# Kernel tuning notes

Hardware: AMD Instinct MI355X
Metric: run time of the kernel (lower is better)

The kernel has to match this reference:

```python
import jax, jax.numpy as jnp
import numpy as np

B, E, W, HID, HOR = 16, 128, 256, 64, 12
EPS = 1e-5


def conv1d(x, w, b, stride=1, padding=0, groups=1):
    # x: [N, Cin, L], w: [Cout, Cin//groups, K]
    y = jax.lax.conv_general_dilated(x, w, (stride,), [(padding, padding)],
                                     feature_group_count=groups,
                                     dimension_numbers=('NCH', 'OIH', 'NCH'))
    return y + b[None, :, None]


def setup_inputs() -> dict:
    key = jax.random.key(0)
    ks = jax.random.split(key, 20)
    def rn(k, shape, scale):
        return jax.random.normal(k, shape, dtype=jnp.float32) * scale
    return {
        'x': rn(ks[0], (B, 1, W), 1.0),
        'noise': rn(ks[1], (HOR, B * E), 1.0),
        'affine_weight': jnp.ones((E,), jnp.float32),
        'affine_bias': jnp.zeros((E,), jnp.float32),
        'pe_w1': rn(ks[2], (32, 1, 5), 1.0 / np.sqrt(5.0)),
        'pe_b1': jnp.zeros((32,), jnp.float32),
        'bn_gamma': jnp.ones((32,), jnp.float32),
        'bn_beta': jnp.zeros((32,), jnp.float32),
        'bn_mean': jnp.zeros((32,), jnp.float32),
        'bn_var': jnp.ones((32,), jnp.float32),
        'pe_w2': rn(ks[3], (E, 32, 1), 1.0 / np.sqrt(32.0)),
        'pe_b2': jnp.zeros((E,), jnp.float32),
        'net_w1': rn(ks[4], (E, 64, 1, 2), 1.0 / np.sqrt(2.0)),
        'net_b1': jnp.zeros((E, 64), jnp.float32),
        'net_w2': rn(ks[5], (E, 64, 4, 2), 1.0 / np.sqrt(8.0)),
        'net_b2': jnp.zeros((E, 64), jnp.float32),
        'net_w3': rn(ks[6], (E, 1, 64, 1), 1.0 / np.sqrt(64.0)),
        'net_b3': jnp.zeros((E, 1), jnp.float32),
        'gat_wl': rn(ks[7], (HID, HID), 1.0 / np.sqrt(HID)),
        'gat_bl': jnp.zeros((HID,), jnp.float32),
        'gat_wr': rn(ks[8], (HID, HID), 1.0 / np.sqrt(HID)),
        'gat_br': jnp.zeros((HID,), jnp.float32),
        'gat_attn': rn(ks[9], (HID,), 1.0 / np.sqrt(HID)),
        'out_w': rn(ks[10], (E, HID), 1.0 / np.sqrt(HID)),
        'out_b': jnp.zeros((E,), jnp.float32),
        'ce_w': rn(ks[11], (HID, 3), 1.0 / np.sqrt(3.0)),
        'ce_b': jnp.zeros((HID,), jnp.float32),
        'cd_w': rn(ks[12], (4, HID), 1.0 / np.sqrt(HID)),
        'cd_b': jnp.zeros((4,), jnp.float32),
        'q_w': rn(ks[13], (32, W), 1.0 / np.sqrt(W)),
        'q_b': jnp.zeros((32,), jnp.float32),
        'k_w': rn(ks[14], (32, W), 1.0 / np.sqrt(W)),
        'k_b': jnp.zeros((32,), jnp.float32),
    }


def reference(x, noise, affine_weight, affine_bias, pe_w1, pe_b1, bn_gamma, bn_beta,
              bn_mean, bn_var, pe_w2, pe_b2, net_w1, net_b1, net_w2, net_b2, net_w3,
              net_b3, gat_wl, gat_bl, gat_wr, gat_br, gat_attn, out_w, out_b,
              ce_w, ce_b, cd_w, cd_b, q_w, q_b, k_w, k_b):
    # instance norm over time axis (unbiased=False, no eps, as in the torch code)
    mean = jnp.mean(x, axis=2, keepdims=True)              # [B,1,1]
    std = jnp.sqrt(jnp.var(x, axis=2, keepdims=True))
    xn = (x - mean) / std

    # path_encoder: conv(1->32,k5,p2) + ReLU + BN(eval) + conv(32->E,k1)
    h0 = jax.nn.relu(conv1d(xn, pe_w1, pe_b1, padding=2))
    h0 = (h0 - bn_mean[None, :, None]) / jnp.sqrt(bn_var + EPS)[None, :, None]
    h0 = h0 * bn_gamma[None, :, None] + bn_beta[None, :, None]
    xf = conv1d(h0, pe_w2, pe_b2)                          # [B,E,W]
    xf = xf * affine_weight[None, :, None] + affine_bias[None, :, None]

    # adjacency learner: softmax(Q K^T) over nodes, then hard threshold
    q = jnp.einsum('bew,hw->beh', xf, q_w) + q_b           # [B,E,32]
    k = jnp.einsum('bew,hw->beh', xf, k_w) + k_b
    adj_soft = jax.nn.softmax(jnp.einsum('bih,bjh->bij', q, k), axis=-1)  # [B,E,E]
    adj_bin = (adj_soft > 0.5).astype(jnp.float32)

    def cnn1d(xc, w1, b1, w2, b2, w3, b3):
        # xc: [B,1,W] -> [B,1,HID]; kernel=stride=down_factor//2=2
        h1 = jnp.tanh(conv1d(xc, w1, b1, stride=2))
        h2 = jnp.tanh(conv1d(h1, w2, b2, stride=2, groups=16))
        return jnp.tanh(conv1d(h2, w3, b3))

    vcnn = jax.vmap(cnn1d, in_axes=(0, 0, 0, 0, 0, 0, 0))

    def gat(h, adj):
        # GATv2, single head, is_concat: e[b,i,j] = a^T lrelu(g_r[i]+g_l[j])
        gl = jnp.einsum('bnf,of->bno', h, gat_wl) + gat_bl   # [B,N,HID]
        gr = jnp.einsum('bnf,of->bno', h, gat_wr) + gat_br
        gs = gr[:, :, None, :] + gl[:, None, :, :]           # [B,N,N,HID]
        e = jnp.einsum('bijf,f->bij', jax.nn.leaky_relu(gs, 0.2), gat_attn)
        e = jnp.where(adj == 0, jnp.float32(-1e20), e)
        a = jax.nn.softmax(e, axis=2)
        return jnp.einsum('bij,bjf->bif', a, gr)             # [B,N,HID]

    def mech(Q_t, P_t, adj, nz):
        Hh, Ee, Vv = Q_t[:, 0], Q_t[:, 1], Q_t[:, 2]
        al, be, ga, et = P_t[:, 0], P_t[:, 1], P_t[:, 2], P_t[:, 3]
        E_coup = jnp.einsum('bij,bj->bi', adj, Ee.reshape(B, E)).reshape(B * E)
        H_new = Hh - al * Hh
        E_new = Ee + be * Hh - ga * Ee + 0.1 * E_coup
        V_new = Vv + et * Ee + nz * 0.01
        return jnp.stack([H_new, E_new, V_new], axis=1)

    Q0 = jnp.tile(jnp.array([1.0, 0.0, 0.0], jnp.float32), (B * E, 1))

    def step(carry, nz):
        xc, Q_t = carry
        xper = xc.transpose(1, 0, 2)[:, :, None, :]          # [E,B,1,W]
        h = vcnn(xper, net_w1, net_b1, net_w2, net_b2, net_w3, net_b3)
        h = h[:, :, 0, :].transpose(1, 0, 2)                 # [B,E,HID]
        h_temp = gat(h, adj_bin)
        H_causal = jnp.tanh(Q_t @ ce_w.T + ce_b).reshape(B, E, HID)
        h = h + jnp.tanh(h_temp) + H_causal
        x_pred = jnp.einsum('beh,eh->be', h, out_w) + out_b  # grouped conv == per-node dot
        x_new = jnp.concatenate([xc[:, :, 1:], x_pred[:, :, None]], axis=2)
        P_t = jax.nn.sigmoid(h.reshape(B * E, HID) @ cd_w.T + cd_b)
        Q_new = mech(Q_t, P_t, adj_bin, nz)
        return (x_new, Q_new), (x_pred, P_t)

    (_, Q_final), (x_preds, P_all) = jax.lax.scan(step, (xf, Q0), noise)
    x_pred_all = x_preds.transpose(1, 2, 0)                  # [B,E,HOR]
    out = (x_pred_all - affine_bias[None, :, None]) / affine_weight[None, :, None]
    out = out * std + mean
    return out, Q_final.reshape(B, E, 3), P_all[-1].reshape(B, E, 4), adj_soft
```

## Files before the change

kernel.cpp:

```cpp
#include <hip/hip_runtime.h>


typedef __attribute__((ext_vector_type(4))) float f32x4;

struct Params {
  const float *__restrict__ x, *__restrict__ noise, *__restrict__ aw, *__restrict__ ab,
              *__restrict__ pe_w1, *__restrict__ pe_b1, *__restrict__ bn_g, *__restrict__ bn_b,
              *__restrict__ bn_m, *__restrict__ bn_v, *__restrict__ pe_w2, *__restrict__ pe_b2,
              *__restrict__ w1, *__restrict__ b1, *__restrict__ w2, *__restrict__ b2,
              *__restrict__ w3, *__restrict__ b3, *__restrict__ wl, *__restrict__ bl,
              *__restrict__ wr, *__restrict__ br, *__restrict__ attn, *__restrict__ out_w,
              *__restrict__ out_b, *__restrict__ ce_w, *__restrict__ ce_b, *__restrict__ cd_w,
              *__restrict__ cd_b, *__restrict__ q_w, *__restrict__ q_b, *__restrict__ k_w,
              *__restrict__ k_b;
  float* ws;
  float* out;
};

__device__ __forceinline__ float fast_tanh(float x) {
  float t = exp2f(fminf(2.8853900818f * x, 126.0f));
  return 1.0f - 2.0f * __builtin_amdgcn_rcpf(t + 1.0f);
}
__device__ __forceinline__ float fast_sigmoid(float x) {
  float t = exp2f(fminf(-1.44269504f * x, 126.0f));
  return __builtin_amdgcn_rcpf(1.0f + t);
}
__device__ __forceinline__ float wsum(float v) {
  #pragma unroll
  for (int m = 1; m < 64; m <<= 1) v += __shfl_xor(v, m, 64);
  return v;
}
__device__ __forceinline__ float wmax(float v) {
  #pragma unroll
  for (int m = 1; m < 64; m <<= 1) v = fmaxf(v, __shfl_xor(v, m, 64));
  return v;
}
__device__ __forceinline__ float load_llc(const float* p) {
  return __hip_atomic_load(p, __ATOMIC_RELAXED, __HIP_MEMORY_SCOPE_AGENT);
}
__device__ __forceinline__ void store_llc(float* p, float v) {
  __hip_atomic_store(p, v, __ATOMIC_RELAXED, __HIP_MEMORY_SCOPE_AGENT);
}
__device__ __forceinline__ f32x4 load_llc4(const float* p) {
  f32x4 v;
  asm volatile("global_load_dwordx4 %0, %1, off sc0 sc1" : "=v"(v) : "v"(p));
  return v;
}
__device__ __forceinline__ float load_llc1(const float* p) {
  float v;
  asm volatile("global_load_dword %0, %1, off sc0 sc1" : "=v"(v) : "v"(p));
  return v;
}
__device__ __forceinline__ void lds_fence() {
  asm volatile("s_waitcnt lgkmcnt(0)" ::: "memory");
  __builtin_amdgcn_sched_barrier(0);
}

#define OFF_MS   0
#define OFF_EB   32
#define OFF_CNT  4128
#define OFF_QV   16416
#define OFF_KV   81952
#define OFF_GL   147488
#define OFF_GR   409632
#define OFF_H0   671776
#define OFF_XW   802848
#define OFF_G    1359904

__global__ __launch_bounds__(256)
void k1_h0(Params P) {
  __shared__ float red[8];
  const int tid = threadIdx.x, blk = blockIdx.x;
  const int idx = blk * 256 + tid;
  const int b = idx >> 13, c = (idx >> 8) & 31, w = idx & 255;
  const int lane = tid & 63, wv = tid >> 6;

  float v = P.x[b * 256 + w];
  float s = wsum(v), s2 = wsum(v * v);
  if (lane == 0) { red[wv] = s; red[4 + wv] = s2; }
  __syncthreads();
  float st  = red[0] + red[1] + red[2] + red[3];
  float st2 = red[4] + red[5] + red[6] + red[7];
  float mean = st * (1.f / 256.f);
  float var  = st2 * (1.f / 256.f) - mean * mean;
  float sd   = sqrtf(var);
  float* ms = P.ws + OFF_MS;
  if (tid == 0) { ms[b] = mean; ms[16 + b] = sd; }

  float rstd = 1.f / sd;
  float acc = P.pe_b1[c];
  #pragma unroll
  for (int k = 0; k < 5; k++) {
    int u = w - 2 + k;
    float xv = (u >= 0 && u < 256) ? (P.x[b * 256 + u] - mean) * rstd : 0.f;
    acc += P.pe_w1[c * 5 + k] * xv;
  }
  acc = fmaxf(acc, 0.f);
  float sc = P.bn_g[c] / sqrtf(P.bn_v[c] + 1e-5f);
  (P.ws + OFF_H0)[idx] = (acc - P.bn_m[c]) * sc + P.bn_b[c];
}

__global__ __launch_bounds__(256)
void k2_xf(Params P) {
  const int idx = blockIdx.x * 256 + threadIdx.x;
  const int b = idx >> 15, e = (idx >> 8) & 127, w = idx & 255;
  const float* w2p  = P.pe_w2 + e * 32;
  const float* hcol = P.ws + OFF_H0 + b * 8192 + w;
  float acc = P.pe_b2[e];
  #pragma unroll 8
  for (int c = 0; c < 32; c++) acc += w2p[c] * hcol[c * 256];
  acc = acc * P.aw[e] + P.ab[e];
  (P.ws + OFF_XW)[(b * 128 + e) * 272 + w] = acc;
}

__global__ __launch_bounds__(256)
void k3_G(Params P) {
  const int row = blockIdx.x;
  const int es  = row & 127;
  const int s   = threadIdx.x;
  const float* w1p = P.w1 + es * 128;
  const float* w2p = P.w2 + es * 512;
  const float* w3p = P.w3 + es * 64;
  const float* b1p = P.b1 + es * 64;
  const float* b2p = P.b2 + es * 64;
  const float  b3v = P.b3[es];
  const float* xr  = P.ws + OFF_XW + row * 272;
  if (s >= 253) return;
  float X0 = xr[s], X1 = xr[s + 1], X2 = xr[s + 2], X3 = xr[s + 3];
  float acc = 0.f;
  #pragma unroll 1
  for (int g2 = 0; g2 < 16; g2++) {
    float h1v[8];
    #pragma unroll
    for (int ic = 0; ic < 4; ic++) {
      int ch = g2 * 4 + ic;
      float ww0 = w1p[ch * 2], ww1 = w1p[ch * 2 + 1], bb = b1p[ch];
      h1v[ic * 2 + 0] = fast_tanh(bb + ww0 * X0 + ww1 * X1);
      h1v[ic * 2 + 1] = fast_tanh(bb + ww0 * X2 + ww1 * X3);
    }
    #pragma unroll
    for (int oc = 0; oc < 4; oc++) {
      int ch = g2 * 4 + oc;
      const float* wq = w2p + ch * 8;
      float a2 = b2p[ch];
      #pragma unroll
      for (int u = 0; u < 8; u++) a2 += wq[u] * h1v[u];
      acc += w3p[ch] * fast_tanh(a2);
    }
  }
  (P.ws + OFF_G)[row * 272 + s] = fast_tanh(b3v + acc);
}

__global__ __launch_bounds__(256)
void k4_qk(Params P) {
  const int gtid = blockIdx.x * 256 + threadIdx.x;
  if (gtid < 16) ((int*)(P.ws + OFF_CNT))[gtid * 32] = 0;
  const int half = gtid >> 16;
  const int idx  = gtid & 65535;
  const int row  = idx >> 5, h = idx & 31;
  const float* wm  = half ? P.k_w : P.q_w;
  const float* bv  = half ? P.k_b : P.q_b;
  const float* xr  = P.ws + OFF_XW + row * 272;
  const float* wrw = wm + h * 256;
  float acc = bv[h];
  #pragma unroll 8
  for (int w = 0; w < 256; w += 4) {
    float4 xx = *(const float4*)(xr + w);
    float4 wq = *(const float4*)(wrw + w);
    acc += xx.x * wq.x + xx.y * wq.y + xx.z * wq.z + xx.w * wq.w;
  }
  ((half ? P.ws + OFF_KV : P.ws + OFF_QV))[idx] = acc;
}

__global__ __launch_bounds__(1024, 4)
void k_scan(Params P) {
  __shared__ __align__(16) float glS_[8192];
  __shared__ __align__(16) float grTS_[8192];
  __shared__ __align__(16) float WlS_[4096];
  __shared__ __align__(16) float WrS_[4096];
  __shared__ __align__(16) float wscb[16 * 336];
  __shared__ __align__(16) float attnS[64];
  const int tid = threadIdx.x, lane = tid & 63, wv = tid >> 6;
  const int row = blockIdx.x * 16 + wv;
  const int b = row >> 7, e = row & 127;
  float* ws = P.ws;
  float* abuf = wscb + wv * 336;
  float* hb   = abuf + 128;
  float* h1b  = abuf + 192;
  float* hist = abuf + 320;
  const float4* hb4   = (const float4*)hb;
  const float4* abuf4 = (const float4*)abuf;
  const float4* attn4 = (const float4*)attnS;
  char* glS  = (char*)glS_;
  char* grTS = (char*)grTS_;
  char* WlSc = (char*)WlS_;
  char* WrSc = (char*)WrS_;
  const float* grow_G = ws + OFF_G + row * 272;
  int* cntb = (int*)(ws + OFF_CNT) + b * 32;

  {
    int o = tid >> 4, q = tid & 15;
    float4 vl = *(const float4*)(P.wl + o * 64 + q * 4);
    float4 vr = *(const float4*)(P.wr + o * 64 + q * 4);
    int off = o * 256 + ((q ^ (o & 15)) << 4);
    *(float4*)(WlSc + off) = vl;
    *(float4*)(WrSc + off) = vr;
  }
  if (tid < 64) attnS[tid] = P.attn[tid];

  float cew0 = P.ce_w[lane * 3], cew1 = P.ce_w[lane * 3 + 1], cew2 = P.ce_w[lane * 3 + 2];
  float cebv = P.ce_b[lane];
  float cdw0 = P.cd_w[lane], cdw1 = P.cd_w[64 + lane], cdw2 = P.cd_w[128 + lane], cdw3 = P.cd_w[192 + lane];
  float cdb0 = P.cd_b[0], cdb1 = P.cd_b[1], cdb2 = P.cd_b[2], cdb3 = P.cd_b[3];
  float outw = P.out_w[e * 64 + lane], outb = P.out_b[e];
  float blv = P.bl[lane], brv = P.br[lane];
  float awv = P.aw[e], abv = P.ab[e];
  float meanb = ws[OFF_MS + b], stdb = ws[OFF_MS + 16 + b];
  float w10 = P.w1[e * 128 + lane * 2], w11 = P.w1[e * 128 + lane * 2 + 1];
  float b1v = P.b1[e * 64 + lane], b2v = P.b2[e * 64 + lane];
  float w3v = P.w3[e * 64 + lane], b3c = P.b3[e];
  float w2r[8];
  {
    const float4* w24 = (const float4*)(P.w2 + e * 512 + lane * 8);
    float4 a = w24[0], c = w24[1];
    w2r[0] = a.x; w2r[1] = a.y; w2r[2] = a.z; w2r[3] = a.w;
    w2r[4] = c.x; w2r[5] = c.y; w2r[6] = c.z; w2r[7] = c.w;
  }

  bool a0b, a1b;
  {
    if (lane < 32) hb[lane] = (ws + OFF_QV)[row * 32 + lane];
    lds_fence();
    float e0, e1;
    #pragma unroll
    for (int half = 0; half < 2; half++) {
      int j = lane + half * 64;
      const float* kr = ws + OFF_KV + (b * 128 + j) * 32;
      float acc = 0.f;
      #pragma unroll
      for (int h = 0; h < 32; h += 4) {
        float4 kk = *(const float4*)(kr + h);
        float4 qq = *(const float4*)(hb + h);
        acc += qq.x * kk.x + qq.y * kk.y + qq.z * kk.z + qq.w * kk.w;
      }
      if (half == 0) e0 = acc; else e1 = acc;
    }
    float m   = wmax(fmaxf(e0, e1));
    float p0  = __expf(e0 - m), p1 = __expf(e1 - m);
    float inv = 1.f / wsum(p0 + p1);
    float av0 = p0 * inv, av1 = p1 * inv;
    P.out[38912 + row * 128 + lane]      = av0;
    P.out[38912 + row * 128 + lane + 64] = av1;
    a0b = av0 > 0.5f; a1b = av1 > 0.5f;
  }

  float h_own = grow_G[4 * lane];
  float xA = (ws + OFF_XW)[row * 272 + 253];
  float xB = (ws + OFF_XW)[row * 272 + 254];
  float xC = (ws + OFF_XW)[row * 272 + 255];
  float q0 = 1.f, q1 = 0.f, q2 = 0.f;
  if (lane == 0) store_llc(ws + OFF_EB + row, 0.f);

  __syncthreads();

  hb[lane] = h_own;
  lds_fence();
  float gri;
  {
    float glx = blv, grx = brv;
    const int k = lane & 15;
    #pragma unroll
    for (int q = 0; q < 16; q++) {
      float4 hq  = hb4[q];
      float4 wl4 = *(const float4*)(WlSc + lane * 256 + ((q ^ k) << 4));
      float4 wr4 = *(const float4*)(WrSc + lane * 256 + ((q ^ k) << 4));
      glx += hq.x * wl4.x + hq.y * wl4.y + hq.z * wl4.z + hq.w * wl4.w;
      grx += hq.x * wr4.x + hq.y * wr4.y + hq.z * wr4.z + hq.w * wr4.w;
    }
    store_llc(ws + OFF_GL + row * 64 + lane, glx);
    store_llc(ws + OFF_GR + b * 8192 + lane * 128 + e, grx);
    gri = grx;
  }

  #pragma unroll 1
  for (int t = 0; t < 12; t++) {
    asm volatile("s_waitcnt vmcnt(0)" ::: "memory");
    __syncthreads();
    if (tid == 0) {
      __hip_atomic_fetch_add(cntb, 1, __ATOMIC_RELAXED, __HIP_MEMORY_SCOPE_AGENT);
      const int target = (t + 1) * 8;
      while (__hip_atomic_load(cntb, __ATOMIC_RELAXED, __HIP_MEMORY_SCOPE_AGENT) < target)
        __builtin_amdgcn_s_sleep(2);
    }
    __syncthreads();

    const float* glG   = ws + OFF_GL + (t & 1) * 131072 + b * 8192;
    const float* grTG  = ws + OFF_GR + (t & 1) * 131072 + b * 8192;
    const float* EbO   = ws + OFF_EB + (t & 1) * 2048;
    float*       EbN   = ws + OFF_EB + ((t + 1) & 1) * 2048;
    float*       glGn  = ws + OFF_GL + ((t + 1) & 1) * 131072;
    float*       grTGn = ws + OFF_GR + ((t + 1) & 1) * 131072;

    float ebv0 = load_llc1(EbO + b * 128 + lane);
    float ebv1 = load_llc1(EbO + b * 128 + lane + 64);
    const int jj0 = tid >> 4, cc0 = tid & 15;
    const int jj1 = 64 + jj0;
    const int ff0 = tid >> 5, dd0 = tid & 31;
    const int ff1 = 32 + ff0;
    f32x4 vg0 = load_llc4(glG  + jj0 * 64  + cc0 * 4);
    f32x4 vg1 = load_llc4(glG  + jj1 * 64  + cc0 * 4);
    f32x4 vr0 = load_llc4(grTG + ff0 * 128 + dd0 * 4);
    f32x4 vr1 = load_llc4(grTG + ff1 * 128 + dd0 * 4);

    asm volatile("s_waitcnt vmcnt(2)" ::: "memory");
    __builtin_amdgcn_sched_barrier(0);
    *(f32x4*)(glS + jj0 * 256 + ((cc0 ^ (jj0 & 15)) << 4)) = vg0;
    *(f32x4*)(glS + jj1 * 256 + ((cc0 ^ (jj1 & 15)) << 4)) = vg1;
    hb[lane] = gri;
    asm volatile("s_waitcnt lgkmcnt(0)" ::: "memory");
    __builtin_amdgcn_sched_barrier(0);
    __builtin_amdgcn_s_barrier();

    float ev0 = 0.f, ev1 = 0.f;
    {
      const char* r0 = glS + lane * 256;
      const char* r1 = glS + (lane + 64) * 256;
      const int k = lane & 15;
      #pragma unroll
      for (int c = 0; c < 16; c++) {
        float4 hq = hb4[c];
        float4 aq = attn4[c];
        int off = (c ^ k) << 4;
        float4 g0 = *(const float4*)(r0 + off);
        float4 g1 = *(const float4*)(r1 + off);
        float v;
        v = hq.x + g0.x; ev0 += fmaxf(v, 0.2f * v) * aq.x;
        v = hq.y + g0.y; ev0 += fmaxf(v, 0.2f * v) * aq.y;
        v = hq.z + g0.z; ev0 += fmaxf(v, 0.2f * v) * aq.z;
        v = hq.w + g0.w; ev0 += fmaxf(v, 0.2f * v) * aq.w;
        v = hq.x + g1.x; ev1 += fmaxf(v, 0.2f * v) * aq.x;
        v = hq.y + g1.y; ev1 += fmaxf(v, 0.2f * v) * aq.y;
        v = hq.z + g1.z; ev1 += fmaxf(v, 0.2f * v) * aq.z;
        v = hq.w + g1.w; ev1 += fmaxf(v, 0.2f * v) * aq.w;
      }
    }

    asm volatile("s_waitcnt vmcnt(0)" ::: "memory");
    __builtin_amdgcn_sched_barrier(0);
    *(f32x4*)(grTS + ff0 * 512 + ((dd0 ^ (ff0 & 15)) << 4)) = vr0;
    *(f32x4*)(grTS + ff1 * 512 + ((dd0 ^ (ff1 & 15)) << 4)) = vr1;

    ev0 = a0b ? ev0 : -1e20f;
    ev1 = a1b ? ev1 : -1e20f;
    float m   = wmax(fmaxf(ev0, ev1));
    float p0  = __expf(ev0 - m), p1 = __expf(ev1 - m);
    float inv = 1.f / wsum(p0 + p1);
    abuf[lane]      = p0 * inv;
    abuf[lane + 64] = p1 * inv;
    __syncthreads();

    float ht = 0.f;
    {
      const char* rr = grTS + lane * 512;
      const int k = lane & 15;
      #pragma unroll
      for (int c = 0; c < 32; c++) {
        float4 aq = abuf4[c];
        float4 g  = *(const float4*)(rr + ((c ^ k) << 4));
        ht += aq.x * g.x + aq.y * g.y + aq.z * g.z + aq.w * g.w;
      }
    }

    float hc = fast_tanh(cebv + q0 * cew0 + q1 * cew1 + q2 * cew2);
    float hf = h_own + fast_tanh(ht) + hc;

    float xp = wsum(hf * outw) + outb;
    float d0 = wsum(hf * cdw0);
    float d1 = wsum(hf * cdw1);
    float d2 = wsum(hf * cdw2);
    float d3 = wsum(hf * cdw3);
    float al = fast_sigmoid(d0 + cdb0);
    float be = fast_sigmoid(d1 + cdb1);
    float ga = fast_sigmoid(d2 + cdb2);
    float et = fast_sigmoid(d3 + cdb3);

    float ec = (a0b ? ebv0 : 0.f) + (a1b ? ebv1 : 0.f);
    ec = wsum(ec);

    float Hn = q0 - al * q0;
    float En = q1 + be * q0 - ga * q1 + 0.1f * ec;
    float Vn = q2 + et * q1 + P.noise[t * 2048 + row] * 0.01f;
    q0 = Hn; q1 = En; q2 = Vn;
    if (lane == 0) {
      store_llc(EbN + row, En);
      P.out[row * 12 + t] = (xp - abv) / awv * stdb + meanb;
      if (t == 11) {
        P.out[24576 + row * 3]     = Hn;
        P.out[24576 + row * 3 + 1] = En;
        P.out[24576 + row * 3 + 2] = Vn;
        P.out[30720 + row * 4]     = al;
        P.out[30720 + row * 4 + 1] = be;
        P.out[30720 + row * 4 + 2] = ga;
        P.out[30720 + row * 4 + 3] = et;
      }
    }

    if (t < 11) {
      float X0 = xA, X1 = xB, X2 = xC, X3 = xp;
      xA = xB; xB = xC; xC = xp;
      float h1a = fast_tanh(b1v + w10 * X0 + w11 * X1);
      float h1c = fast_tanh(b1v + w10 * X2 + w11 * X3);
      h1b[lane * 2]     = h1a;
      h1b[lane * 2 + 1] = h1c;
      lds_fence();
      const float* h1g = h1b + (lane >> 2) * 8;
      float a2 = b2v;
      #pragma unroll
      for (int u = 0; u < 8; u++) a2 += w2r[u] * h1g[u];
      float h2v = fast_tanh(a2);
      float g3  = wsum(w3v * h2v);
      float Gn  = fast_tanh(b3c + g3);
      if (lane == 0) hist[t] = Gn;

      float hnext;
      if (lane == 63) {
        hnext = Gn;
      } else {
        int gi = (t + 1) + 4 * lane;
        hnext = (gi >= 253) ? hist[gi - 253] : grow_G[gi];
      }
      hb[lane] = hnext;
      lds_fence();
      float glx = blv, grx = brv;
      const int k = lane & 15;
      #pragma unroll
      for (int q = 0; q < 16; q++) {
        float4 hq  = hb4[q];
        float4 wl4 = *(const float4*)(WlSc + lane * 256 + ((q ^ k) << 4));
        float4 wr4 = *(const float4*)(WrSc + lane * 256 + ((q ^ k) << 4));
        glx += hq.x * wl4.x + hq.y * wl4.y + hq.z * wl4.z + hq.w * wl4.w;
        grx += hq.x * wr4.x + hq.y * wr4.y + hq.z * wr4.z + hq.w * wr4.w;
      }
      store_llc(glGn + row * 64 + lane, glx);
      store_llc(grTGn + b * 8192 + lane * 128 + e, grx);
      gri = grx;
      h_own = hnext;
    }
  }
}

extern "C" void kernel_launch(void* const* d_in, const int* in_sizes, int n_in,
                              void* d_out, int out_size, void* d_ws, size_t ws_size,
                              hipStream_t stream) {
  Params p;
  p.x     = (const float*)d_in[0];  p.noise = (const float*)d_in[1];
  p.aw    = (const float*)d_in[2];  p.ab    = (const float*)d_in[3];
  p.pe_w1 = (const float*)d_in[4];  p.pe_b1 = (const float*)d_in[5];
  p.bn_g  = (const float*)d_in[6];  p.bn_b  = (const float*)d_in[7];
  p.bn_m  = (const float*)d_in[8];  p.bn_v  = (const float*)d_in[9];
  p.pe_w2 = (const float*)d_in[10]; p.pe_b2 = (const float*)d_in[11];
  p.w1    = (const float*)d_in[12]; p.b1    = (const float*)d_in[13];
  p.w2    = (const float*)d_in[14]; p.b2    = (const float*)d_in[15];
  p.w3    = (const float*)d_in[16]; p.b3    = (const float*)d_in[17];
  p.wl    = (const float*)d_in[18]; p.bl    = (const float*)d_in[19];
  p.wr    = (const float*)d_in[20]; p.br    = (const float*)d_in[21];
  p.attn  = (const float*)d_in[22]; p.out_w = (const float*)d_in[23];
  p.out_b = (const float*)d_in[24]; p.ce_w  = (const float*)d_in[25];
  p.ce_b  = (const float*)d_in[26]; p.cd_w  = (const float*)d_in[27];
  p.cd_b  = (const float*)d_in[28]; p.q_w   = (const float*)d_in[29];
  p.q_b   = (const float*)d_in[30]; p.k_w   = (const float*)d_in[31];
  p.k_b   = (const float*)d_in[32];
  p.ws  = (float*)d_ws;
  p.out = (float*)d_out;

  k1_h0<<<dim3(512),  dim3(256), 0, stream>>>(p);
  k2_xf<<<dim3(2048), dim3(256), 0, stream>>>(p);
  k3_G <<<dim3(2048), dim3(256), 0, stream>>>(p);
  k4_qk<<<dim3(512),  dim3(256), 0, stream>>>(p);
  k_scan<<<dim3(128), dim3(1024), 0, stream>>>(p);
}
```

Baseline: 270.2 us.

## Exchange GAT projections as bf16 in scan and merge k3/k4 launches

The per-step cross-block exchange of the gl and grT projections now writes and reads bf16 instead of fp32. This halves global and LDS traffic on the serial scan's critical path and shrinks the LDS staging buffers. Separately, the G-precompute and Q/K projection kernels are merged into one launch to save a kernel boundary. The bf16 rounding adds precision loss to the attention scores and the aggregation, which may drift over the 12-step recurrence.

```diff
diff --git a/kernel.cpp b/kernel.cpp
--- a/kernel.cpp
+++ b/kernel.cpp
@@ -41,7 +41,10 @@
 __device__ __forceinline__ void store_llc(float* p, float v) {
   __hip_atomic_store(p, v, __ATOMIC_RELAXED, __HIP_MEMORY_SCOPE_AGENT);
 }
-__device__ __forceinline__ f32x4 load_llc4(const float* p) {
+__device__ __forceinline__ void store_llc_u32(unsigned* p, unsigned v) {
+  __hip_atomic_store(p, v, __ATOMIC_RELAXED, __HIP_MEMORY_SCOPE_AGENT);
+}
+__device__ __forceinline__ f32x4 load_llc4(const void* p) {
   f32x4 v;
   asm volatile("global_load_dwordx4 %0, %1, off sc0 sc1" : "=v"(v) : "v"(p));
   return v;
@@ -51,6 +54,15 @@
   asm volatile("global_load_dword %0, %1, off sc0 sc1" : "=v"(v) : "v"(p));
   return v;
 }
+__device__ __forceinline__ void store_llc_u16(void* p, unsigned v) {
+  asm volatile("global_store_short %0, %1, off sc0 sc1" :: "v"(p), "v"(v) : "memory");
+}
+__device__ __forceinline__ unsigned to_bf16(float f) {
+  unsigned u = __float_as_uint(f);
+  return (u + 0x7fffu + ((u >> 16) & 1u)) >> 16;
+}
+__device__ __forceinline__ float blo(unsigned w) { return __uint_as_float(w << 16); }
+__device__ __forceinline__ float bhi(unsigned w) { return __uint_as_float(w & 0xffff0000u); }
 __device__ __forceinline__ void lds_fence() {
   asm volatile("s_waitcnt lgkmcnt(0)" ::: "memory");
   __builtin_amdgcn_sched_barrier(0);
@@ -114,68 +126,67 @@
 }
 
 __global__ __launch_bounds__(256)
-void k3_G(Params P) {
-  const int row = blockIdx.x;
-  const int es  = row & 127;
-  const int s   = threadIdx.x;
-  const float* w1p = P.w1 + es * 128;
-  const float* w2p = P.w2 + es * 512;
-  const float* w3p = P.w3 + es * 64;
-  const float* b1p = P.b1 + es * 64;
-  const float* b2p = P.b2 + es * 64;
-  const float  b3v = P.b3[es];
-  const float* xr  = P.ws + OFF_XW + row * 272;
-  if (s >= 253) return;
-  float X0 = xr[s], X1 = xr[s + 1], X2 = xr[s + 2], X3 = xr[s + 3];
-  float acc = 0.f;
-  #pragma unroll 1
-  for (int g2 = 0; g2 < 16; g2++) {
-    float h1v[8];
-    #pragma unroll
-    for (int ic = 0; ic < 4; ic++) {
-      int ch = g2 * 4 + ic;
-      float ww0 = w1p[ch * 2], ww1 = w1p[ch * 2 + 1], bb = b1p[ch];
-      h1v[ic * 2 + 0] = fast_tanh(bb + ww0 * X0 + ww1 * X1);
-      h1v[ic * 2 + 1] = fast_tanh(bb + ww0 * X2 + ww1 * X3);
-    }
-    #pragma unroll
-    for (int oc = 0; oc < 4; oc++) {
-      int ch = g2 * 4 + oc;
-      const float* wq = w2p + ch * 8;
-      float a2 = b2p[ch];
-      #pragma unroll
-      for (int u = 0; u < 8; u++) a2 += wq[u] * h1v[u];
-      acc += w3p[ch] * fast_tanh(a2);
-    }
-  }
-  (P.ws + OFF_G)[row * 272 + s] = fast_tanh(b3v + acc);
-}
-
-__global__ __launch_bounds__(256)
-void k4_qk(Params P) {
-  const int gtid = blockIdx.x * 256 + threadIdx.x;
-  if (gtid < 16) ((int*)(P.ws + OFF_CNT))[gtid * 32] = 0;
-  const int half = gtid >> 16;
-  const int idx  = gtid & 65535;
-  const int row  = idx >> 5, h = idx & 31;
-  const float* wm  = half ? P.k_w : P.q_w;
-  const float* bv  = half ? P.k_b : P.q_b;
-  const float* xr  = P.ws + OFF_XW + row * 272;
-  const float* wrw = wm + h * 256;
-  float acc = bv[h];
-  #pragma unroll 8
-  for (int w = 0; w < 256; w += 4) {
-    float4 xx = *(const float4*)(xr + w);
-    float4 wq = *(const float4*)(wrw + w);
-    acc += xx.x * wq.x + xx.y * wq.y + xx.z * wq.z + xx.w * wq.w;
-  }
-  ((half ? P.ws + OFF_KV : P.ws + OFF_QV))[idx] = acc;
+void k34(Params P) {
+  if (blockIdx.x < 2048) {
+    const int row = blockIdx.x;
+    const int es  = row & 127;
+    const int s   = threadIdx.x;
+    const float* w1p = P.w1 + es * 128;
+    const float* w2p = P.w2 + es * 512;
+    const float* w3p = P.w3 + es * 64;
+    const float* b1p = P.b1 + es * 64;
+    const float* b2p = P.b2 + es * 64;
+    const float  b3v = P.b3[es];
+    const float* xr  = P.ws + OFF_XW + row * 272;
+    if (s >= 253) return;
+    float X0 = xr[s], X1 = xr[s + 1], X2 = xr[s + 2], X3 = xr[s + 3];
+    float acc = 0.f;
+    #pragma unroll 1
+    for (int g2 = 0; g2 < 16; g2++) {
+      float h1v[8];
+      #pragma unroll
+      for (int ic = 0; ic < 4; ic++) {
+        int ch = g2 * 4 + ic;
+        float ww0 = w1p[ch * 2], ww1 = w1p[ch * 2 + 1], bb = b1p[ch];
+        h1v[ic * 2 + 0] = fast_tanh(bb + ww0 * X0 + ww1 * X1);
+        h1v[ic * 2 + 1] = fast_tanh(bb + ww0 * X2 + ww1 * X3);
+      }
+      #pragma unroll
+      for (int oc = 0; oc < 4; oc++) {
+        int ch = g2 * 4 + oc;
+        const float* wq = w2p + ch * 8;
+        float a2 = b2p[ch];
+        #pragma unroll
+        for (int u = 0; u < 8; u++) a2 += wq[u] * h1v[u];
+        acc += w3p[ch] * fast_tanh(a2);
+      }
+    }
+    (P.ws + OFF_G)[row * 272 + s] = fast_tanh(b3v + acc);
+  } else {
+    const int gtid = (blockIdx.x - 2048) * 256 + threadIdx.x;
+    if (gtid < 16) ((int*)(P.ws + OFF_CNT))[gtid * 32] = 0;
+    const int half = gtid >> 16;
+    const int idx  = gtid & 65535;
+    const int row  = idx >> 5, h = idx & 31;
+    const float* wm  = half ? P.k_w : P.q_w;
+    const float* bv  = half ? P.k_b : P.q_b;
+    const float* xr  = P.ws + OFF_XW + row * 272;
+    const float* wrw = wm + h * 256;
+    float acc = bv[h];
+    #pragma unroll 8
+    for (int w = 0; w < 256; w += 4) {
+      float4 xx = *(const float4*)(xr + w);
+      float4 wq = *(const float4*)(wrw + w);
+      acc += xx.x * wq.x + xx.y * wq.y + xx.z * wq.z + xx.w * wq.w;
+    }
+    ((half ? P.ws + OFF_KV : P.ws + OFF_QV))[idx] = acc;
+  }
 }
 
 __global__ __launch_bounds__(1024, 4)
 void k_scan(Params P) {
-  __shared__ __align__(16) float glS_[8192];
-  __shared__ __align__(16) float grTS_[8192];
+  __shared__ __align__(16) char  glS[16384];
+  __shared__ __align__(16) char  grTS[16384];
   __shared__ __align__(16) float WlS_[4096];
   __shared__ __align__(16) float WrS_[4096];
   __shared__ __align__(16) float wscb[16 * 336];
@@ -191,8 +202,6 @@
   const float4* hb4   = (const float4*)hb;
   const float4* abuf4 = (const float4*)abuf;
   const float4* attn4 = (const float4*)attnS;
-  char* glS  = (char*)glS_;
-  char* grTS = (char*)grTS_;
   char* WlSc = (char*)WlS_;
   char* WrSc = (char*)WrS_;
   const float* grow_G = ws + OFF_G + row * 272;
@@ -277,8 +286,13 @@
       glx += hq.x * wl4.x + hq.y * wl4.y + hq.z * wl4.z + hq.w * wl4.w;
       grx += hq.x * wr4.x + hq.y * wr4.y + hq.z * wr4.z + hq.w * wr4.w;
     }
-    store_llc(ws + OFF_GL + row * 64 + lane, glx);
-    store_llc(ws + OFF_GR + b * 8192 + lane * 128 + e, grx);
+    char* glB  = (char*)(ws + OFF_GL) + b * 32768;
+    char* grTB = (char*)(ws + OFF_GR) + b * 32768;
+    unsigned ub = to_bf16(glx);
+    unsigned pb = (unsigned)__shfl_xor((int)ub, 1, 64);
+    if (!(lane & 1))
+      store_llc_u32((unsigned*)(glB + e * 128) + (lane >> 1), ub | (pb << 16));
+    store_llc_u16(grTB + lane * 256 + e * 2, to_bf16(grx));
     gri = grx;
   }
 
@@ -294,28 +308,23 @@
     }
     __syncthreads();
 
-    const float* glG   = ws + OFF_GL + (t & 1) * 131072 + b * 8192;
-    const float* grTG  = ws + OFF_GR + (t & 1) * 131072 + b * 8192;
-    const float* EbO   = ws + OFF_EB + (t & 1) * 2048;
-    float*       EbN   = ws + OFF_EB + ((t + 1) & 1) * 2048;
-    float*       glGn  = ws + OFF_GL + ((t + 1) & 1) * 131072;
-    float*       grTGn = ws + OFF_GR + ((t + 1) & 1) * 131072;
+    const char* glG   = (const char*)(ws + OFF_GL + (t & 1) * 131072) + b * 32768;
+    const char* grTG  = (const char*)(ws + OFF_GR + (t & 1) * 131072) + b * 32768;
+    const float* EbO  = ws + OFF_EB + (t & 1) * 2048;
+    float*       EbN  = ws + OFF_EB + ((t + 1) & 1) * 2048;
+    char*        glGn  = (char*)(ws + OFF_GL + ((t + 1) & 1) * 131072) + b * 32768;
+    char*        grTGn = (char*)(ws + OFF_GR + ((t + 1) & 1) * 131072) + b * 32768;
 
     float ebv0 = load_llc1(EbO + b * 128 + lane);
     float ebv1 = load_llc1(EbO + b * 128 + lane + 64);
-    const int jj0 = tid >> 4, cc0 = tid & 15;
-    const int jj1 = 64 + jj0;
-    const int ff0 = tid >> 5, dd0 = tid & 31;
-    const int ff1 = 32 + ff0;
-    f32x4 vg0 = load_llc4(glG  + jj0 * 64  + cc0 * 4);
-    f32x4 vg1 = load_llc4(glG  + jj1 * 64  + cc0 * 4);
-    f32x4 vr0 = load_llc4(grTG + ff0 * 128 + dd0 * 4);
-    f32x4 vr1 = load_llc4(grTG + ff1 * 128 + dd0 * 4);
-
-    asm volatile("s_waitcnt vmcnt(2)" ::: "memory");
+    const int jj = tid >> 3, jc = tid & 7;
+    const int ff = tid >> 4, fc = tid & 15;
+    f32x4 vg = load_llc4(glG  + jj * 128 + jc * 16);
+    f32x4 vr = load_llc4(grTG + ff * 256 + fc * 16);
+
+    asm volatile("s_waitcnt vmcnt(1)" ::: "memory");
     __builtin_amdgcn_sched_barrier(0);
-    *(f32x4*)(glS + jj0 * 256 + ((cc0 ^ (jj0 & 15)) << 4)) = vg0;
-    *(f32x4*)(glS + jj1 * 256 + ((cc0 ^ (jj1 & 15)) << 4)) = vg1;
+    *(f32x4*)(glS + jj * 128 + ((jc ^ (jj & 7)) << 4)) = vg;
     hb[lane] = gri;
     asm volatile("s_waitcnt lgkmcnt(0)" ::: "memory");
     __builtin_amdgcn_sched_barrier(0);
@@ -323,32 +332,39 @@
 
     float ev0 = 0.f, ev1 = 0.f;
     {
-      const char* r0 = glS + lane * 256;
-      const char* r1 = glS + (lane + 64) * 256;
-      const int k = lane & 15;
-      #pragma unroll
-      for (int c = 0; c < 16; c++) {
-        float4 hq = hb4[c];
-        float4 aq = attn4[c];
+      const char* r0 = glS + lane * 128;
+      const char* r1 = glS + (lane + 64) * 128;
+      const int k = lane & 7;
+      #pragma unroll
+      for (int c = 0; c < 8; c++) {
+        float4 hqA = hb4[2 * c], hqB = hb4[2 * c + 1];
+        float4 aqA = attn4[2 * c], aqB = attn4[2 * c + 1];
         int off = (c ^ k) << 4;
-        float4 g0 = *(const float4*)(r0 + off);
-        float4 g1 = *(const float4*)(r1 + off);
+        uint4 g0 = *(const uint4*)(r0 + off);
+        uint4 g1 = *(const uint4*)(r1 + off);
         float v;
-        v = hq.x + g0.x; ev0 += fmaxf(v, 0.2f * v) * aq.x;
-        v = hq.y + g0.y; ev0 += fmaxf(v, 0.2f * v) * aq.y;
-        v = hq.z + g0.z; ev0 += fmaxf(v, 0.2f * v) * aq.z;
-        v = hq.w + g0.w; ev0 += fmaxf(v, 0.2f * v) * aq.w;
-        v = hq.x + g1.x; ev1 += fmaxf(v, 0.2f * v) * aq.x;
-        v = hq.y + g1.y; ev1 += fmaxf(v, 0.2f * v) * aq.y;
-        v = hq.z + g1.z; ev1 += fmaxf(v, 0.2f * v) * aq.z;
-        v = hq.w + g1.w; ev1 += fmaxf(v, 0.2f * v) * aq.w;
+        v = hqA.x + blo(g0.x); ev0 += fmaxf(v, 0.2f * v) * aqA.x;
+        v = hqA.y + bhi(g0.x); ev0 += fmaxf(v, 0.2f * v) * aqA.y;
+        v = hqA.z + blo(g0.y); ev0 += fmaxf(v, 0.2f * v) * aqA.z;
+        v = hqA.w + bhi(g0.y); ev0 += fmaxf(v, 0.2f * v) * aqA.w;
+        v = hqB.x + blo(g0.z); ev0 += fmaxf(v, 0.2f * v) * aqB.x;
+        v = hqB.y + bhi(g0.z); ev0 += fmaxf(v, 0.2f * v) * aqB.y;
+        v = hqB.z + blo(g0.w); ev0 += fmaxf(v, 0.2f * v) * aqB.z;
+        v = hqB.w + bhi(g0.w); ev0 += fmaxf(v, 0.2f * v) * aqB.w;
+        v = hqA.x + blo(g1.x); ev1 += fmaxf(v, 0.2f * v) * aqA.x;
+        v = hqA.y + bhi(g1.x); ev1 += fmaxf(v, 0.2f * v) * aqA.y;
+        v = hqA.z + blo(g1.y); ev1 += fmaxf(v, 0.2f * v) * aqA.z;
+        v = hqA.w + bhi(g1.y); ev1 += fmaxf(v, 0.2f * v) * aqA.w;
+        v = hqB.x + blo(g1.z); ev1 += fmaxf(v, 0.2f * v) * aqB.x;
+        v = hqB.y + bhi(g1.z); ev1 += fmaxf(v, 0.2f * v) * aqB.y;
+        v = hqB.z + blo(g1.w); ev1 += fmaxf(v, 0.2f * v) * aqB.z;
+        v = hqB.w + bhi(g1.w); ev1 += fmaxf(v, 0.2f * v) * aqB.w;
       }
     }
 
     asm volatile("s_waitcnt vmcnt(0)" ::: "memory");
     __builtin_amdgcn_sched_barrier(0);
-    *(f32x4*)(grTS + ff0 * 512 + ((dd0 ^ (ff0 & 15)) << 4)) = vr0;
-    *(f32x4*)(grTS + ff1 * 512 + ((dd0 ^ (ff1 & 15)) << 4)) = vr1;
+    *(f32x4*)(grTS + ff * 256 + ((fc ^ (ff & 15)) << 4)) = vr;
 
     ev0 = a0b ? ev0 : -1e20f;
     ev1 = a1b ? ev1 : -1e20f;
@@ -361,13 +377,14 @@
 
     float ht = 0.f;
     {
-      const char* rr = grTS + lane * 512;
+      const char* rr = grTS + lane * 256;
       const int k = lane & 15;
       #pragma unroll
-      for (int c = 0; c < 32; c++) {
-        float4 aq = abuf4[c];
-        float4 g  = *(const float4*)(rr + ((c ^ k) << 4));
-        ht += aq.x * g.x + aq.y * g.y + aq.z * g.z + aq.w * g.w;
+      for (int c = 0; c < 16; c++) {
+        float4 aA = abuf4[2 * c], aB = abuf4[2 * c + 1];
+        uint4 g = *(const uint4*)(rr + ((c ^ k) << 4));
+        ht += aA.x * blo(g.x) + aA.y * bhi(g.x) + aA.z * blo(g.y) + aA.w * bhi(g.y)
+            + aB.x * blo(g.z) + aB.y * bhi(g.z) + aB.z * blo(g.w) + aB.w * bhi(g.w);
       }
     }
 
@@ -441,8 +458,11 @@
         glx += hq.x * wl4.x + hq.y * wl4.y + hq.z * wl4.z + hq.w * wl4.w;
         grx += hq.x * wr4.x + hq.y * wr4.y + hq.z * wr4.z + hq.w * wr4.w;
       }
-      store_llc(glGn + row * 64 + lane, glx);
-      store_llc(grTGn + b * 8192 + lane * 128 + e, grx);
+      unsigned ub = to_bf16(glx);
+      unsigned pb = (unsigned)__shfl_xor((int)ub, 1, 64);
+      if (!(lane & 1))
+        store_llc_u32((unsigned*)(glGn + e * 128) + (lane >> 1), ub | (pb << 16));
+      store_llc_u16(grTGn + lane * 256 + e * 2, to_bf16(grx));
       gri = grx;
       h_own = hnext;
     }
@@ -475,7 +495,6 @@
 
   k1_h0<<<dim3(512),  dim3(256), 0, stream>>>(p);
   k2_xf<<<dim3(2048), dim3(256), 0, stream>>>(p);
-  k3_G <<<dim3(2048), dim3(256), 0, stream>>>(p);
-  k4_qk<<<dim3(512),  dim3(256), 0, stream>>>(p);
+  k34  <<<dim3(2560), dim3(256), 0, stream>>>(p);
   k_scan<<<dim3(128), dim3(1024), 0, stream>>>(p);
 }
```

After: 438.5 us. 1.62x slower.
